# Performance work log

Hardware: AMD Instinct MI355X
Metric: run time of the kernel (lower is better)

Reference implementation:

```python
import jax, jax.numpy as jnp
import numpy as np

N_NODES = 100000
N_EDGES = 1600000
N_GRAPHS = 512
IN_F, H1, H2 = 128, 128, 256
N_GROUPS, N_FAM = 16, 10


def setup_inputs() -> dict:
    key = jax.random.key(0)
    ks = jax.random.split(key, 8)
    x = jax.random.normal(ks[0], (N_NODES, IN_F), dtype=jnp.float32)
    edge_index = jax.random.randint(ks[1], (2, N_EDGES), 0, N_NODES, dtype=jnp.int64)
    batch = jnp.sort(jax.random.randint(ks[2], (N_NODES,), 0, N_GRAPHS, dtype=jnp.int64))
    W1 = jax.random.normal(ks[3], (IN_F, H1), dtype=jnp.float32) / np.sqrt(IN_F)
    b1 = jnp.zeros((H1,), dtype=jnp.float32)
    W2 = jax.random.normal(ks[4], (H1, H2), dtype=jnp.float32) / np.sqrt(H1)
    b2 = jnp.zeros((H2,), dtype=jnp.float32)
    Wg = jax.random.normal(ks[5], (H2, N_GROUPS), dtype=jnp.float32) / np.sqrt(H2)
    bg = jnp.zeros((N_GROUPS,), dtype=jnp.float32)
    Wf = jax.random.normal(ks[6], (N_GROUPS, H2, N_FAM), dtype=jnp.float32) / np.sqrt(H2)
    bf = jnp.zeros((N_GROUPS, N_FAM), dtype=jnp.float32)
    return {"x": x, "edge_index": edge_index, "batch": batch,
            "W1": W1, "b1": b1, "W2": W2, "b2": b2,
            "Wg": Wg, "bg": bg, "Wf": Wf, "bf": bf}


def gcn_conv(x, W, b, src, dst, num_nodes):
    # PyG GCNConv: add self-loops, symmetric normalization, scatter-add aggregation.
    xw = x @ W  # [N, out]
    deg = jax.ops.segment_sum(jnp.ones((src.shape[0],), x.dtype), dst,
                              num_segments=num_nodes) + 1.0  # +1 self-loop
    dinv = jax.lax.rsqrt(deg)
    coef = dinv[src] * dinv[dst]            # [E]
    msg = xw[src] * coef[:, None]           # gather + scale (memory-bound)
    agg = jax.ops.segment_sum(msg, dst, num_segments=num_nodes)
    agg = agg + xw * (dinv * dinv)[:, None]  # self-loop contribution
    return agg + b


def reference(x, edge_index, batch, W1, b1, W2, b2, Wg, bg, Wf, bf):
    src, dst = edge_index[0], edge_index[1]
    h = jax.nn.relu(gcn_conv(x, W1, b1, src, dst, N_NODES))
    # dropout p=0.5 is identity in eval mode
    h = gcn_conv(h, W2, b2, src, dst, N_NODES)
    # global mean pool over graphs
    sums = jax.ops.segment_sum(h, batch, num_segments=N_GRAPHS)       # [G, H2]
    cnts = jax.ops.segment_sum(jnp.ones((N_NODES,), h.dtype), batch,
                               num_segments=N_GRAPHS)
    pooled = sums / jnp.maximum(cnts, 1.0)[:, None]
    group_logits = pooled @ Wg + bg                                   # [G, num_groups]
    family_logits = jnp.einsum('bd,gdf->gbf', pooled, Wf) + bf[:, None, :]
    return group_logits, family_logits
```

## Files before the change

kernel.cpp:

```cpp
#include <hip/hip_runtime.h>

#define NN 100000
#define NE 1600000
#define NGR 512
#define KF 128
#define H2F 256
#define NGRP 16
#define NFAM 10

#define CH 128
#define NCHUNK ((NN + CH - 1) / CH)
#define PT 6656
#define NT ((NE + PT - 1) / PT)

typedef __attribute__((ext_vector_type(8))) short short8;
typedef __attribute__((ext_vector_type(4))) float floatx4;

__device__ __forceinline__ unsigned short f2bf(float f) {
  unsigned u = __float_as_uint(f);
  unsigned r = (u + 0x7fff + ((u >> 16) & 1)) >> 16;
  return (unsigned short)r;
}
__device__ __forceinline__ float2 bf2f(unsigned u) {
  float2 r;
  r.x = __uint_as_float(u << 16);
  r.y = __uint_as_float(u & 0xffff0000u);
  return r;
}


__global__ __launch_bounds__(256) void k_phist(const int* __restrict__ ei,
                                               int* __restrict__ mat) {
  __shared__ int lh[NCHUNK];
  int t0 = blockIdx.x, tid = threadIdx.x;
  for (int g = tid; g < NCHUNK; g += 256) lh[g] = 0;
  __syncthreads();
  int base = t0 * PT;
  int nv = min(PT, NE - base);
  for (int i = tid; i < nv; i += 256) atomicAdd(&lh[ei[NE + base + i] >> 7], 1);
  __syncthreads();
  for (int g = tid; g < NCHUNK; g += 256) mat[t0 * NCHUNK + g] = lh[g];
}

__global__ __launch_bounds__(256) void k_colsum(const int* __restrict__ mat,
                                                int* __restrict__ tot) {
  int g = blockIdx.x * 4 + (threadIdx.x >> 6);
  if (g >= NCHUNK) return;
  int lane = threadIdx.x & 63;
  int s = 0;
  for (int t = lane; t < NT; t += 64) s += mat[t * NCHUNK + g];
#pragma unroll
  for (int off = 32; off > 0; off >>= 1) s += __shfl_down(s, off);
  if (lane == 0) tot[g] = s;
}

__global__ __launch_bounds__(256) void k_scantot(const int* __restrict__ tot,
                                                 int* __restrict__ cbase) {
  __shared__ int ssc[256];
  int tid = threadIdx.x;
  int v4[4]; int loc = 0;
#pragma unroll
  for (int j = 0; j < 4; ++j) {
    int idx = tid * 4 + j;
    v4[j] = (idx < NCHUNK) ? tot[idx] : 0;
    loc += v4[j];
  }
  ssc[tid] = loc;
  __syncthreads();
  for (int off = 1; off < 256; off <<= 1) {
    int val = (tid >= off) ? ssc[tid - off] : 0;
    __syncthreads();
    ssc[tid] += val;
    __syncthreads();
  }
  int excl = ssc[tid] - loc;
#pragma unroll
  for (int j = 0; j < 4; ++j) {
    int idx = tid * 4 + j;
    if (idx < NCHUNK) cbase[idx] = excl;
    excl += v4[j];
  }
  if (tid == 255) cbase[NCHUNK] = excl;
}

__global__ __launch_bounds__(256) void k_colfix(int* __restrict__ mat,
                                                const int* __restrict__ cbase) {
  int g = blockIdx.x * 4 + (threadIdx.x >> 6);
  if (g >= NCHUNK) return;
  int lane = threadIdx.x & 63;
  int v[4]; int loc = 0;
#pragma unroll
  for (int j = 0; j < 4; ++j) {
    int t = lane * 4 + j;
    v[j] = (t < NT) ? mat[t * NCHUNK + g] : 0;
    loc += v[j];
  }
  int incl = loc;
#pragma unroll
  for (int off = 1; off < 64; off <<= 1) {
    int o = __shfl_up(incl, off);
    if (lane >= off) incl += o;
  }
  int excl = incl - loc + cbase[g];
#pragma unroll
  for (int j = 0; j < 4; ++j) {
    int t = lane * 4 + j;
    if (t < NT) mat[t * NCHUNK + g] = excl;
    excl += v[j];
  }
}

__global__ __launch_bounds__(256) void k_pscatter(const int* __restrict__ ei,
                                                  const int* __restrict__ mat,
                                                  int2* __restrict__ erec) {
  __shared__ int2 stage[PT];
  __shared__ int lstart[NCHUNK];
  __shared__ int lrun[NCHUNK];
  __shared__ int loff[NCHUNK];
  __shared__ int ssc[256];
  int t0 = blockIdx.x, tid = threadIdx.x;
  for (int g = tid; g < NCHUNK; g += 256) lrun[g] = 0;
  __syncthreads();
  int base = t0 * PT;
  int nv = min(PT, NE - base);
  for (int i = tid; i < nv; i += 256) atomicAdd(&lrun[ei[NE + base + i] >> 7], 1);
  __syncthreads();
  int v4[4]; int loc = 0;
#pragma unroll
  for (int j = 0; j < 4; ++j) {
    int idx = tid * 4 + j;
    v4[j] = (idx < NCHUNK) ? lrun[idx] : 0;
    loc += v4[j];
  }
  ssc[tid] = loc;
  __syncthreads();
  for (int off = 1; off < 256; off <<= 1) {
    int val = (tid >= off) ? ssc[tid - off] : 0;
    __syncthreads();
    ssc[tid] += val;
    __syncthreads();
  }
  int excl = ssc[tid] - loc;
#pragma unroll
  for (int j = 0; j < 4; ++j) {
    int idx = tid * 4 + j;
    if (idx < NCHUNK) lstart[idx] = excl;
    excl += v4[j];
  }
  __syncthreads();
  for (int g = tid; g < NCHUNK; g += 256) {
    lrun[g] = lstart[g];
    loff[g] = mat[t0 * NCHUNK + g];
  }
  __syncthreads();
  for (int i = tid; i < nv; i += 256) {
    int s = ei[base + i], d = ei[NE + base + i];
    int pos = atomicAdd(&lrun[d >> 7], 1);
    stage[pos] = make_int2(s, d);
  }
  __syncthreads();
  for (int j = tid; j < nv; j += 256) {
    int2 r = stage[j];
    int g = r.y >> 7;
    erec[loff[g] + (j - lstart[g])] = r;
  }
}


__global__ __launch_bounds__(256) void k_sort(const int2* __restrict__ erec,
                                              const int* __restrict__ cbase,
                                              int* __restrict__ esrc,
                                              int* __restrict__ rowptr,
                                              float* __restrict__ dinv) {
  __shared__ int hist[CH];
  __shared__ int lrun[CH];
  __shared__ int sc[256];
  const int c = blockIdx.x, tid = threadIdx.x;
  const int e0 = cbase[c], e1 = cbase[c + 1];
  const int nv = e1 - e0;
  if (tid < CH) hist[tid] = 0;
  __syncthreads();
  for (int i = tid; i < nv; i += 256) atomicAdd(&hist[erec[e0 + i].y & (CH - 1)], 1);
  __syncthreads();
  int deg = (tid < CH) ? hist[tid] : 0;
  sc[tid] = deg;
  __syncthreads();
  for (int off = 1; off < 256; off <<= 1) {
    int val = (tid >= off) ? sc[tid - off] : 0;
    __syncthreads();
    sc[tid] += val;
    __syncthreads();
  }
  int excl = sc[tid] - deg;
  int node = c * CH + tid;
  if (tid < CH) {
    lrun[tid] = excl;
    if (node < NN) {
      rowptr[node] = e0 + excl;
      dinv[node] = rsqrtf((float)(deg + 1));
    } else if (node == NN) {
      rowptr[NN] = e0 + excl;
    }
  }
  __syncthreads();
  for (int i = tid; i < nv; i += 256) {
    int2 r = erec[e0 + i];
    int pos = atomicAdd(&lrun[r.y & (CH - 1)], 1);
    esrc[e0 + pos] = r.x;
  }
}


__global__ void k_prepB(const float* __restrict__ W, unsigned short* __restrict__ Bp,
                        int Ncol) {
  int idx = blockIdx.x * 256 + threadIdx.x;
  int total = 128 * Ncol;
  if (idx >= total) return;
  int NCH = Ncol >> 4;
  int j = idx & 7;
  int l = (idx >> 3) & 63;
  int rest = idx >> 9;
  int nc = rest % NCH;
  int kc = rest / NCH;
  int k = kc * 32 + (l >> 4) * 8 + j;
  int nn = nc * 16 + (l & 15);
  Bp[idx] = f2bf(W[k * Ncol + nn]);
}


__global__ __launch_bounds__(256) void k_gemm_mfma(const float* __restrict__ A,
                                                   const unsigned short* __restrict__ Bp,
                                                   const float* __restrict__ dinv,
                                                   unsigned short* __restrict__ C) {
  constexpr int K = 128;
  constexpr int N = KF;
  constexpr int NCH = N / 16;
  const int wv = blockIdx.x * 4 + (threadIdx.x >> 6);
  const int row0 = wv * 16;
  if (row0 >= NN) return;
  const int lane = threadIdx.x & 63;
  const int m = lane & 15;
  const int q = lane >> 4;

  floatx4 acc[NCH];
#pragma unroll
  for (int i = 0; i < NCH; ++i) acc[i] = (floatx4){0.f, 0.f, 0.f, 0.f};

  const int arow = row0 + m;
#pragma unroll
  for (int kc = 0; kc < 4; ++kc) {
    const float* ap = A + (size_t)arow * K + kc * 32 + q * 8;
    float4 f0 = *(const float4*)ap;
    float4 f1 = *(const float4*)(ap + 4);
    short8 af;
    af[0] = (short)f2bf(f0.x); af[1] = (short)f2bf(f0.y);
    af[2] = (short)f2bf(f0.z); af[3] = (short)f2bf(f0.w);
    af[4] = (short)f2bf(f1.x); af[5] = (short)f2bf(f1.y);
    af[6] = (short)f2bf(f1.z); af[7] = (short)f2bf(f1.w);
    const unsigned short* bp = Bp + (size_t)kc * NCH * 512;
#pragma unroll
    for (int nc = 0; nc < NCH; ++nc) {
      short8 bfr = *(const short8*)(bp + (size_t)nc * 512 + lane * 8);
      acc[nc] = __builtin_amdgcn_mfma_f32_16x16x32_bf16(af, bfr, acc[nc], 0, 0, 0);
    }
  }

  float ds[4];
#pragma unroll
  for (int r = 0; r < 4; ++r) ds[r] = dinv[row0 + q * 4 + r];
#pragma unroll
  for (int nc = 0; nc < NCH; ++nc) {
#pragma unroll
    for (int r = 0; r < 4; ++r) {
      int row = row0 + q * 4 + r;
      C[(size_t)row * N + nc * 16 + m] = f2bf(acc[nc][r] * ds[r]);
    }
  }
}


template <bool FIRST>
__global__ __launch_bounds__(128) void k_agg(const unsigned* __restrict__ p,
                                             const float* __restrict__ bias,
                                             const int* __restrict__ rowptr,
                                             const int* __restrict__ esrc,
                                             const float* __restrict__ dinv,
                                             unsigned* __restrict__ out) {
  const int n = blockIdx.x * 2 + (threadIdx.x >> 6);
  const int t = threadIdx.x & 63;

  float2 f = bf2f(p[(size_t)n * 64 + t]);
  float ax = f.x, ay = f.y;

  const int r0 = rowptr[n];
  const int r1 = rowptr[n + 1];
  int i = r0;
  for (; i + 8 <= r1; i += 8) {
    int s0 = esrc[i], s1 = esrc[i + 1], s2 = esrc[i + 2], s3 = esrc[i + 3];
    int s4 = esrc[i + 4], s5 = esrc[i + 5], s6 = esrc[i + 6], s7 = esrc[i + 7];
    unsigned u0 = p[(size_t)s0 * 64 + t];
    unsigned u1 = p[(size_t)s1 * 64 + t];
    unsigned u2 = p[(size_t)s2 * 64 + t];
    unsigned u3 = p[(size_t)s3 * 64 + t];
    unsigned u4 = p[(size_t)s4 * 64 + t];
    unsigned u5 = p[(size_t)s5 * 64 + t];
    unsigned u6 = p[(size_t)s6 * 64 + t];
    unsigned u7 = p[(size_t)s7 * 64 + t];
    f = bf2f(u0); ax += f.x; ay += f.y;
    f = bf2f(u1); ax += f.x; ay += f.y;
    f = bf2f(u2); ax += f.x; ay += f.y;
    f = bf2f(u3); ax += f.x; ay += f.y;
    f = bf2f(u4); ax += f.x; ay += f.y;
    f = bf2f(u5); ax += f.x; ay += f.y;
    f = bf2f(u6); ax += f.x; ay += f.y;
    f = bf2f(u7); ax += f.x; ay += f.y;
  }
  for (; i + 4 <= r1; i += 4) {
    int s0 = esrc[i], s1 = esrc[i + 1], s2 = esrc[i + 2], s3 = esrc[i + 3];
    unsigned u0 = p[(size_t)s0 * 64 + t];
    unsigned u1 = p[(size_t)s1 * 64 + t];
    unsigned u2 = p[(size_t)s2 * 64 + t];
    unsigned u3 = p[(size_t)s3 * 64 + t];
    f = bf2f(u0); ax += f.x; ay += f.y;
    f = bf2f(u1); ax += f.x; ay += f.y;
    f = bf2f(u2); ax += f.x; ay += f.y;
    f = bf2f(u3); ax += f.x; ay += f.y;
  }
  for (; i < r1; ++i) {
    int s = esrc[i];
    f = bf2f(p[(size_t)s * 64 + t]);
    ax += f.x; ay += f.y;
  }

  const float dn = dinv[n];
  if (FIRST) {
    float2 bb = ((const float2*)bias)[t];
    ax = fmaf(dn, ax, bb.x);
    ay = fmaf(dn, ay, bb.y);
    ax = fmaxf(ax, 0.f) * dn;
    ay = fmaxf(ay, 0.f) * dn;
  } else {
    ax *= dn;
    ay *= dn;
  }
  out[(size_t)n * 64 + t] = (unsigned)f2bf(ax) | ((unsigned)f2bf(ay) << 16);
}


__global__ __launch_bounds__(256) void k_pool(const unsigned* __restrict__ p,
                                              const int* __restrict__ batch,
                                              float* __restrict__ pooled_raw) {
  int g = blockIdx.x;
  int t = threadIdx.x & 63;
  int wv = threadIdx.x >> 6;
  int lo = 0, hi = NN;
  while (lo < hi) { int mid = (lo + hi) >> 1; if (batch[mid] < g) lo = mid + 1; else hi = mid; }
  int start = lo;
  hi = NN;
  while (lo < hi) { int mid = (lo + hi) >> 1; if (batch[mid] < g + 1) lo = mid + 1; else hi = mid; }
  int end = lo;

  float sx = 0.f, sy = 0.f;
  int n = start + wv;
  for (; n + 12 < end; n += 16) {
    unsigned u0 = p[(size_t)n * 64 + t];
    unsigned u1 = p[(size_t)(n + 4) * 64 + t];
    unsigned u2 = p[(size_t)(n + 8) * 64 + t];
    unsigned u3 = p[(size_t)(n + 12) * 64 + t];
    float2 f0 = bf2f(u0), f1 = bf2f(u1), f2 = bf2f(u2), f3 = bf2f(u3);
    sx += (f0.x + f1.x) + (f2.x + f3.x);
    sy += (f0.y + f1.y) + (f2.y + f3.y);
  }
  for (; n < end; n += 4) {
    float2 f = bf2f(p[(size_t)n * 64 + t]);
    sx += f.x; sy += f.y;
  }

  __shared__ float sh[4][128];
  sh[wv][2 * t] = sx;
  sh[wv][2 * t + 1] = sy;
  __syncthreads();
  if (wv == 0) {
    float vx = sh[0][2 * t] + sh[1][2 * t] + sh[2][2 * t] + sh[3][2 * t];
    float vy = sh[0][2 * t + 1] + sh[1][2 * t + 1] + sh[2][2 * t + 1] + sh[3][2 * t + 1];
    float c = fmaxf((float)(end - start), 1.f);
    pooled_raw[g * KF + 2 * t] = vx / c;
    pooled_raw[g * KF + 2 * t + 1] = vy / c;
  }
}


__global__ __launch_bounds__(256) void k_heads(const float* __restrict__ praw,
                                               const float* __restrict__ W2,
                                               const float* __restrict__ b2,
                                               const float* __restrict__ Wg,
                                               const float* __restrict__ bg,
                                               const float* __restrict__ Wf,
                                               const float* __restrict__ bfb,
                                               float* __restrict__ out) {
  int b = blockIdx.x;
  int t = threadIdx.x;
  __shared__ float pr[KF];
  __shared__ float p[H2F];
  if (t < KF) pr[t] = praw[b * KF + t];
  __syncthreads();
  float acc = b2[t];
#pragma unroll 8
  for (int d = 0; d < KF; ++d) acc = fmaf(pr[d], W2[d * H2F + t], acc);
  p[t] = acc;
  __syncthreads();
  if (t < NGRP) {
    float a = bg[t];
    for (int d = 0; d < H2F; ++d) a = fmaf(p[d], Wg[d * NGRP + t], a);
    out[b * NGRP + t] = a;
  } else if (t >= 64 && t < 64 + NGRP * NFAM) {
    int u = t - 64;
    int g = u / NFAM;
    int ff = u % NFAM;
    float a = bfb[g * NFAM + ff];
    for (int d = 0; d < H2F; ++d) a = fmaf(p[d], Wf[(g * H2F + d) * NFAM + ff], a);
    out[NGR * NGRP + (size_t)g * NGR * NFAM + b * NFAM + ff] = a;
  }
}


extern "C" void kernel_launch(void* const* d_in, const int* in_sizes, int n_in,
                              void* d_out, int out_size, void* d_ws, size_t ws_size,
                              hipStream_t stream) {
  const float* x    = (const float*)d_in[0];
  const int*   ei   = (const int*)d_in[1];
  const int*   batch= (const int*)d_in[2];
  const float* W1   = (const float*)d_in[3];
  const float* b1   = (const float*)d_in[4];
  const float* W2   = (const float*)d_in[5];
  const float* b2   = (const float*)d_in[6];
  const float* Wg   = (const float*)d_in[7];
  const float* bg   = (const float*)d_in[8];
  const float* Wf   = (const float*)d_in[9];
  const float* bfb  = (const float*)d_in[10];
  float* out = (float*)d_out;

  char* w = (char*)d_ws;
  auto take = [&](size_t bytes) {
    char* p = w;
    w += (bytes + 255) & ~(size_t)255;
    return (void*)p;
  };
  int*   mat   = (int*)take((size_t)NT * NCHUNK * 4);
  int*   tot   = (int*)take((size_t)NCHUNK * 4);
  int*   cbase = (int*)take((size_t)(NCHUNK + 1) * 4);
  int2*  erec  = (int2*)take((size_t)NT * PT * 8);
  int*   esrc  = (int*)take((size_t)NE * 4);
  int*   rowptr= (int*)take((size_t)(NN + 1) * 4);
  float* dinv  = (float*)take((size_t)NN * 4);
  float* praw  = (float*)take((size_t)NGR * KF * 4);
  unsigned short* Bp1 = (unsigned short*)take((size_t)KF * KF * 2);
  unsigned* xw1 = (unsigned*)take((size_t)NN * KF * 2);
  unsigned* h1  = (unsigned*)take((size_t)NN * KF * 2);
  unsigned* agg2= (unsigned*)take((size_t)NN * KF * 2);

  k_phist<<<NT, 256, 0, stream>>>(ei, mat);
  k_colsum<<<(NCHUNK + 3) / 4, 256, 0, stream>>>(mat, tot);
  k_scantot<<<1, 256, 0, stream>>>(tot, cbase);
  k_colfix<<<(NCHUNK + 3) / 4, 256, 0, stream>>>(mat, cbase);
  k_pscatter<<<NT, 256, 0, stream>>>(ei, mat, erec);
  k_sort<<<NCHUNK, 256, 0, stream>>>(erec, cbase, esrc, rowptr, dinv);

  k_prepB<<<(KF * KF + 255) / 256, 256, 0, stream>>>(W1, Bp1, KF);
  k_gemm_mfma<<<1563, 256, 0, stream>>>(x, Bp1, dinv, (unsigned short*)xw1);

  k_agg<true><<<NN / 2, 128, 0, stream>>>(xw1, b1, rowptr, esrc, dinv, h1);
  k_agg<false><<<NN / 2, 128, 0, stream>>>(h1, nullptr, rowptr, esrc, dinv, agg2);

  k_pool<<<NGR, 256, 0, stream>>>(agg2, batch, praw);
  k_heads<<<NGR, 256, 0, stream>>>(praw, W2, b2, Wg, bg, Wf, bfb, out);
}
```

Before: 347.9 us.

## Replace per-tile offset matrix with global atomics and fuse small kernels

The per-tile histogram matrix with its column-sum and column-fix passes is replaced by global atomic accumulation of chunk totals, plus an atomic cursor that hands each scatter tile its base offset per chunk. Weight packing for the first GEMM is merged into the histogram launch as extra blocks, and pooling is fused with the output heads. This removes four kernel launches and the matrix traffic, but adds a memset and global atomic contention. Edge order within a chunk now depends on atomic timing, though the per-node sort in k_sort still groups edges by destination.

```diff
diff --git a/kernel.cpp b/kernel.cpp
--- a/kernel.cpp
+++ b/kernel.cpp
@@ -12,6 +12,7 @@
 #define NCHUNK ((NN + CH - 1) / CH)
 #define PT 6656
 #define NT ((NE + PT - 1) / PT)
+#define PREPB_BLKS 64
 
 typedef __attribute__((ext_vector_type(8))) short short8;
 typedef __attribute__((ext_vector_type(4))) float floatx4;
@@ -29,33 +30,40 @@
 }
 
 
-__global__ __launch_bounds__(256) void k_phist(const int* __restrict__ ei,
-                                               int* __restrict__ mat) {
+__global__ __launch_bounds__(256) void k_histprep(const int* __restrict__ ei,
+                                                  int* __restrict__ tot,
+                                                  const float* __restrict__ W,
+                                                  unsigned short* __restrict__ Bp) {
   __shared__ int lh[NCHUNK];
-  int t0 = blockIdx.x, tid = threadIdx.x;
+  int tid = threadIdx.x;
+  if (blockIdx.x >= NT) {
+    int idx = (blockIdx.x - NT) * 256 + tid;
+    int j = idx & 7;
+    int l = (idx >> 3) & 63;
+    int rest = idx >> 9;
+    int nc = rest & 7;
+    int kc = rest >> 3;
+    int k = kc * 32 + (l >> 4) * 8 + j;
+    int nn = nc * 16 + (l & 15);
+    Bp[idx] = f2bf(W[k * KF + nn]);
+    return;
+  }
   for (int g = tid; g < NCHUNK; g += 256) lh[g] = 0;
   __syncthreads();
-  int base = t0 * PT;
+  int base = blockIdx.x * PT;
   int nv = min(PT, NE - base);
   for (int i = tid; i < nv; i += 256) atomicAdd(&lh[ei[NE + base + i] >> 7], 1);
   __syncthreads();
-  for (int g = tid; g < NCHUNK; g += 256) mat[t0 * NCHUNK + g] = lh[g];
-}
-
-__global__ __launch_bounds__(256) void k_colsum(const int* __restrict__ mat,
-                                                int* __restrict__ tot) {
-  int g = blockIdx.x * 4 + (threadIdx.x >> 6);
-  if (g >= NCHUNK) return;
-  int lane = threadIdx.x & 63;
-  int s = 0;
-  for (int t = lane; t < NT; t += 64) s += mat[t * NCHUNK + g];
-#pragma unroll
-  for (int off = 32; off > 0; off >>= 1) s += __shfl_down(s, off);
-  if (lane == 0) tot[g] = s;
-}
+  for (int g = tid; g < NCHUNK; g += 256) {
+    int v = lh[g];
+    if (v) atomicAdd(&tot[g], v);
+  }
+}
+
 
 __global__ __launch_bounds__(256) void k_scantot(const int* __restrict__ tot,
-                                                 int* __restrict__ cbase) {
+                                                 int* __restrict__ cbase,
+                                                 int* __restrict__ cursor) {
   __shared__ int ssc[256];
   int tid = threadIdx.x;
   int v4[4]; int loc = 0;
@@ -77,46 +85,20 @@
 #pragma unroll
   for (int j = 0; j < 4; ++j) {
     int idx = tid * 4 + j;
-    if (idx < NCHUNK) cbase[idx] = excl;
+    if (idx < NCHUNK) { cbase[idx] = excl; cursor[idx] = excl; }
     excl += v4[j];
   }
   if (tid == 255) cbase[NCHUNK] = excl;
 }
 
-__global__ __launch_bounds__(256) void k_colfix(int* __restrict__ mat,
-                                                const int* __restrict__ cbase) {
-  int g = blockIdx.x * 4 + (threadIdx.x >> 6);
-  if (g >= NCHUNK) return;
-  int lane = threadIdx.x & 63;
-  int v[4]; int loc = 0;
-#pragma unroll
-  for (int j = 0; j < 4; ++j) {
-    int t = lane * 4 + j;
-    v[j] = (t < NT) ? mat[t * NCHUNK + g] : 0;
-    loc += v[j];
-  }
-  int incl = loc;
-#pragma unroll
-  for (int off = 1; off < 64; off <<= 1) {
-    int o = __shfl_up(incl, off);
-    if (lane >= off) incl += o;
-  }
-  int excl = incl - loc + cbase[g];
-#pragma unroll
-  for (int j = 0; j < 4; ++j) {
-    int t = lane * 4 + j;
-    if (t < NT) mat[t * NCHUNK + g] = excl;
-    excl += v[j];
-  }
-}
 
 __global__ __launch_bounds__(256) void k_pscatter(const int* __restrict__ ei,
-                                                  const int* __restrict__ mat,
+                                                  int* __restrict__ cursor,
                                                   int2* __restrict__ erec) {
   __shared__ int2 stage[PT];
   __shared__ int lstart[NCHUNK];
   __shared__ int lrun[NCHUNK];
-  __shared__ int loff[NCHUNK];
+  __shared__ int gbase[NCHUNK];
   __shared__ int ssc[256];
   int t0 = blockIdx.x, tid = threadIdx.x;
   for (int g = tid; g < NCHUNK; g += 256) lrun[g] = 0;
@@ -149,8 +131,9 @@
   }
   __syncthreads();
   for (int g = tid; g < NCHUNK; g += 256) {
+    int cnt = ((g + 1 < NCHUNK) ? lstart[g + 1] : nv) - lstart[g];
+    gbase[g] = cnt ? atomicAdd(&cursor[g], cnt) : 0;
     lrun[g] = lstart[g];
-    loff[g] = mat[t0 * NCHUNK + g];
   }
   __syncthreads();
   for (int i = tid; i < nv; i += 256) {
@@ -162,7 +145,7 @@
   for (int j = tid; j < nv; j += 256) {
     int2 r = stage[j];
     int g = r.y >> 7;
-    erec[loff[g] + (j - lstart[g])] = r;
+    erec[gbase[g] + (j - lstart[g])] = r;
   }
 }
 
@@ -208,23 +191,6 @@
     int pos = atomicAdd(&lrun[r.y & (CH - 1)], 1);
     esrc[e0 + pos] = r.x;
   }
-}
-
-
-__global__ void k_prepB(const float* __restrict__ W, unsigned short* __restrict__ Bp,
-                        int Ncol) {
-  int idx = blockIdx.x * 256 + threadIdx.x;
-  int total = 128 * Ncol;
-  if (idx >= total) return;
-  int NCH = Ncol >> 4;
-  int j = idx & 7;
-  int l = (idx >> 3) & 63;
-  int rest = idx >> 9;
-  int nc = rest % NCH;
-  int kc = rest / NCH;
-  int k = kc * 32 + (l >> 4) * 8 + j;
-  int nn = nc * 16 + (l & 15);
-  Bp[idx] = f2bf(W[k * Ncol + nn]);
 }
 
 
@@ -347,36 +313,46 @@
 }
 
 
-__global__ __launch_bounds__(256) void k_pool(const unsigned* __restrict__ p,
-                                              const int* __restrict__ batch,
-                                              float* __restrict__ pooled_raw) {
-  int g = blockIdx.x;
-  int t = threadIdx.x & 63;
-  int wv = threadIdx.x >> 6;
-  int lo = 0, hi = NN;
-  while (lo < hi) { int mid = (lo + hi) >> 1; if (batch[mid] < g) lo = mid + 1; else hi = mid; }
-  int start = lo;
-  hi = NN;
-  while (lo < hi) { int mid = (lo + hi) >> 1; if (batch[mid] < g + 1) lo = mid + 1; else hi = mid; }
-  int end = lo;
+__global__ __launch_bounds__(256) void k_poolheads(const unsigned* __restrict__ hp,
+                                                   const int* __restrict__ batch,
+                                                   const float* __restrict__ W2,
+                                                   const float* __restrict__ b2,
+                                                   const float* __restrict__ Wg,
+                                                   const float* __restrict__ bg,
+                                                   const float* __restrict__ Wf,
+                                                   const float* __restrict__ bfb,
+                                                   float* __restrict__ out) {
+  __shared__ float sh[4][128];
+  __shared__ float pr[KF];
+  __shared__ float p[H2F];
+  __shared__ int bnd[2];
+  const int g = blockIdx.x;
+  const int tid = threadIdx.x;
+  if (tid < 2) {
+    int target = g + tid;
+    int lo = 0, hi = NN;
+    while (lo < hi) { int mid = (lo + hi) >> 1; if (batch[mid] < target) lo = mid + 1; else hi = mid; }
+    bnd[tid] = lo;
+  }
+  __syncthreads();
+  const int start = bnd[0], end = bnd[1];
+  const int t = tid & 63, wv = tid >> 6;
 
   float sx = 0.f, sy = 0.f;
   int n = start + wv;
   for (; n + 12 < end; n += 16) {
-    unsigned u0 = p[(size_t)n * 64 + t];
-    unsigned u1 = p[(size_t)(n + 4) * 64 + t];
-    unsigned u2 = p[(size_t)(n + 8) * 64 + t];
-    unsigned u3 = p[(size_t)(n + 12) * 64 + t];
+    unsigned u0 = hp[(size_t)n * 64 + t];
+    unsigned u1 = hp[(size_t)(n + 4) * 64 + t];
+    unsigned u2 = hp[(size_t)(n + 8) * 64 + t];
+    unsigned u3 = hp[(size_t)(n + 12) * 64 + t];
     float2 f0 = bf2f(u0), f1 = bf2f(u1), f2 = bf2f(u2), f3 = bf2f(u3);
     sx += (f0.x + f1.x) + (f2.x + f3.x);
     sy += (f0.y + f1.y) + (f2.y + f3.y);
   }
   for (; n < end; n += 4) {
-    float2 f = bf2f(p[(size_t)n * 64 + t]);
+    float2 f = bf2f(hp[(size_t)n * 64 + t]);
     sx += f.x; sy += f.y;
   }
-
-  __shared__ float sh[4][128];
   sh[wv][2 * t] = sx;
   sh[wv][2 * t + 1] = sy;
   __syncthreads();
@@ -384,42 +360,26 @@
     float vx = sh[0][2 * t] + sh[1][2 * t] + sh[2][2 * t] + sh[3][2 * t];
     float vy = sh[0][2 * t + 1] + sh[1][2 * t + 1] + sh[2][2 * t + 1] + sh[3][2 * t + 1];
     float c = fmaxf((float)(end - start), 1.f);
-    pooled_raw[g * KF + 2 * t] = vx / c;
-    pooled_raw[g * KF + 2 * t + 1] = vy / c;
-  }
-}
-
-
-__global__ __launch_bounds__(256) void k_heads(const float* __restrict__ praw,
-                                               const float* __restrict__ W2,
-                                               const float* __restrict__ b2,
-                                               const float* __restrict__ Wg,
-                                               const float* __restrict__ bg,
-                                               const float* __restrict__ Wf,
-                                               const float* __restrict__ bfb,
-                                               float* __restrict__ out) {
-  int b = blockIdx.x;
-  int t = threadIdx.x;
-  __shared__ float pr[KF];
-  __shared__ float p[H2F];
-  if (t < KF) pr[t] = praw[b * KF + t];
-  __syncthreads();
-  float acc = b2[t];
+    pr[2 * t] = vx / c;
+    pr[2 * t + 1] = vy / c;
+  }
+  __syncthreads();
+  float acc = b2[tid];
 #pragma unroll 8
-  for (int d = 0; d < KF; ++d) acc = fmaf(pr[d], W2[d * H2F + t], acc);
-  p[t] = acc;
-  __syncthreads();
-  if (t < NGRP) {
-    float a = bg[t];
-    for (int d = 0; d < H2F; ++d) a = fmaf(p[d], Wg[d * NGRP + t], a);
-    out[b * NGRP + t] = a;
-  } else if (t >= 64 && t < 64 + NGRP * NFAM) {
-    int u = t - 64;
-    int g = u / NFAM;
+  for (int d = 0; d < KF; ++d) acc = fmaf(pr[d], W2[d * H2F + tid], acc);
+  p[tid] = acc;
+  __syncthreads();
+  if (tid < NGRP) {
+    float a = bg[tid];
+    for (int d = 0; d < H2F; ++d) a = fmaf(p[d], Wg[d * NGRP + tid], a);
+    out[g * NGRP + tid] = a;
+  } else if (tid >= 64 && tid < 64 + NGRP * NFAM) {
+    int u = tid - 64;
+    int gg = u / NFAM;
     int ff = u % NFAM;
-    float a = bfb[g * NFAM + ff];
-    for (int d = 0; d < H2F; ++d) a = fmaf(p[d], Wf[(g * H2F + d) * NFAM + ff], a);
-    out[NGR * NGRP + (size_t)g * NGR * NFAM + b * NFAM + ff] = a;
+    float a = bfb[gg * NFAM + ff];
+    for (int d = 0; d < H2F; ++d) a = fmaf(p[d], Wf[(gg * H2F + d) * NFAM + ff], a);
+    out[NGR * NGRP + (size_t)gg * NGR * NFAM + g * NFAM + ff] = a;
   }
 }
 
@@ -446,32 +406,28 @@
     w += (bytes + 255) & ~(size_t)255;
     return (void*)p;
   };
-  int*   mat   = (int*)take((size_t)NT * NCHUNK * 4);
   int*   tot   = (int*)take((size_t)NCHUNK * 4);
   int*   cbase = (int*)take((size_t)(NCHUNK + 1) * 4);
-  int2*  erec  = (int2*)take((size_t)NT * PT * 8);
+  int*   cursor= (int*)take((size_t)NCHUNK * 4);
+  int2*  erec  = (int2*)take((size_t)NE * 8);
   int*   esrc  = (int*)take((size_t)NE * 4);
   int*   rowptr= (int*)take((size_t)(NN + 1) * 4);
   float* dinv  = (float*)take((size_t)NN * 4);
-  float* praw  = (float*)take((size_t)NGR * KF * 4);
   unsigned short* Bp1 = (unsigned short*)take((size_t)KF * KF * 2);
   unsigned* xw1 = (unsigned*)take((size_t)NN * KF * 2);
   unsigned* h1  = (unsigned*)take((size_t)NN * KF * 2);
   unsigned* agg2= (unsigned*)take((size_t)NN * KF * 2);
 
-  k_phist<<<NT, 256, 0, stream>>>(ei, mat);
-  k_colsum<<<(NCHUNK + 3) / 4, 256, 0, stream>>>(mat, tot);
-  k_scantot<<<1, 256, 0, stream>>>(tot, cbase);
-  k_colfix<<<(NCHUNK + 3) / 4, 256, 0, stream>>>(mat, cbase);
-  k_pscatter<<<NT, 256, 0, stream>>>(ei, mat, erec);
+  hipMemsetAsync(tot, 0, (size_t)NCHUNK * 4, stream);
+  k_histprep<<<NT + PREPB_BLKS, 256, 0, stream>>>(ei, tot, W1, Bp1);
+  k_scantot<<<1, 256, 0, stream>>>(tot, cbase, cursor);
+  k_pscatter<<<NT, 256, 0, stream>>>(ei, cursor, erec);
   k_sort<<<NCHUNK, 256, 0, stream>>>(erec, cbase, esrc, rowptr, dinv);
 
-  k_prepB<<<(KF * KF + 255) / 256, 256, 0, stream>>>(W1, Bp1, KF);
   k_gemm_mfma<<<1563, 256, 0, stream>>>(x, Bp1, dinv, (unsigned short*)xw1);
 
   k_agg<true><<<NN / 2, 128, 0, stream>>>(xw1, b1, rowptr, esrc, dinv, h1);
   k_agg<false><<<NN / 2, 128, 0, stream>>>(h1, nullptr, rowptr, esrc, dinv, agg2);
 
-  k_pool<<<NGR, 256, 0, stream>>>(agg2, batch, praw);
-  k_heads<<<NGR, 256, 0, stream>>>(praw, W2, b2, Wg, bg, Wf, bfb, out);
-}
+  k_poolheads<<<NGR, 256, 0, stream>>>(agg2, batch, W2, b2, Wg, bg, Wf, bfb, out);
+}
```

Result: no change. 341.2 us (-1.9%).
